# Optimization experiments

Hardware: AMD Instinct MI355X
Metric: run time of the kernel (lower is better)

The kernel has to match this reference:

```python
import jax, jax.numpy as jnp
import numpy as np


def _bilinear_align_corners(img, H_out, W_out):
    # img: [B, C, h, w] -> [B, C, H_out, W_out], matching F.interpolate(mode='bilinear', align_corners=True)
    b, c, h, w = img.shape
    ys = jnp.linspace(0.0, h - 1.0, H_out)
    xs = jnp.linspace(0.0, w - 1.0, W_out)
    y0 = jnp.floor(ys).astype(jnp.int32)
    x0 = jnp.floor(xs).astype(jnp.int32)
    y1 = jnp.minimum(y0 + 1, h - 1)
    x1 = jnp.minimum(x0 + 1, w - 1)
    wy = (ys - y0)[:, None]          # [H_out, 1]
    wx = (xs - x0)[None, :]          # [1, W_out]

    def gather(yi, xi):
        return img[:, :, yi, :][:, :, :, xi]  # [B, C, H_out, W_out]

    top = gather(y0, x0) * (1.0 - wx) + gather(y0, x1) * wx
    bot = gather(y1, x0) * (1.0 - wx) + gather(y1, x1) * wx
    return top * (1.0 - wy) + bot * wy


def _conv1x1(x, W, b):
    # x: [B, C, H, W_], W: [O, C], b: [O]
    return jnp.einsum('bchw,oc->bohw', x, W) + b[None, :, None, None]


def setup_inputs() -> dict:
    key = jax.random.key(0)
    ks = jax.random.split(key, 9)
    B, C, H, W = 4, 256, 64, 64
    C8 = C // 8
    s_qk = 1.0 / np.sqrt(C)
    return {
        'x': jax.random.normal(ks[0], (B, C, H, W), dtype=jnp.float32),
        'guiding_map0': jax.random.normal(ks[1], (B, 1, 32, 32), dtype=jnp.float32),
        'Wq': jax.random.normal(ks[2], (C8, C), dtype=jnp.float32) * s_qk,
        'bq': jax.random.normal(ks[3], (C8,), dtype=jnp.float32) * 0.01,
        'Wk': jax.random.normal(ks[4], (C8, C), dtype=jnp.float32) * s_qk,
        'bk': jax.random.normal(ks[5], (C8,), dtype=jnp.float32) * 0.01,
        'Wv': jax.random.normal(ks[6], (C, C), dtype=jnp.float32) * s_qk,
        'bv': jax.random.normal(ks[7], (C,), dtype=jnp.float32) * 0.01,
        'gamma': jax.random.normal(ks[8], (1,), dtype=jnp.float32) * 0.1,
    }


def reference(x, guiding_map0, Wq, bq, Wk, bk, Wv, bv, gamma):
    B, C, H, W = x.shape
    N = H * W
    # upsample guiding map to x's spatial size, then sigmoid gate
    gm = jax.nn.sigmoid(_bilinear_align_corners(guiding_map0, H, W))  # [B,1,H,W]
    gate = 1.0 + gm

    q = (_conv1x1(x, Wq, bq) * gate).reshape(B, -1, N)  # [B, C//8, N]
    k = (_conv1x1(x, Wk, bk) * gate).reshape(B, -1, N)  # [B, C//8, N]
    v = (_conv1x1(x, Wv, bv) * gate).reshape(B, C, N)   # [B, C, N]

    # energy[b, n, m] = q[b, :, n] . k[b, :, m]
    energy = jnp.einsum('bcn,bcm->bnm', q, k)           # [B, N, N]
    attention = jax.nn.softmax(energy, axis=-1)
    # out[b, c, n] = sum_m v[b, c, m] * attention[b, n, m]
    out = jnp.einsum('bcm,bnm->bcn', v, attention).reshape(B, C, H, W)
    return gamma[0] * out + x
```

## Files before the change

kernel.cpp:

```cpp
#include <hip/hip_runtime.h>
#include <hip/hip_bf16.h>
#include <cstdint>

typedef __attribute__((ext_vector_type(4)))  float f32x4;
typedef __attribute__((ext_vector_type(16))) float f32x16;
typedef __attribute__((ext_vector_type(8)))  short s16x8;

#define LOG2E 1.4426950408889634f
#define MFIX  64.0f

#define B_   4
#define C_   256
#define N_   4096
#define NT_  256
#define MB_  128
#define QG_  128

#define WS_WFRAG 0u
#define WS_BIAS  163840u
#define WS_Q     262144u
#define WS_K     1310720u
#define WS_V     2359296u
#define WS_PART  11534336u
#define WS_ML    45088768u
#define WS_NEED  45613056ull

__device__ __forceinline__ short bf16s(float f) {
  return (short)__bfloat16_as_ushort(__float2bfloat16(f));
}
__device__ __forceinline__ float bf2f(short h) {
  union { unsigned u; float f; } v; v.u = ((unsigned)(unsigned short)h) << 16;
  return v.f;
}
__device__ __forceinline__ void gl_lds16(const void* g, void* l) {
  __builtin_amdgcn_global_load_lds(
      (const __attribute__((address_space(1))) unsigned int*)g,
      (__attribute__((address_space(3))) unsigned int*)l, 16, 0, 0);
}

__global__ void wprep_kernel(const float* __restrict__ Wq, const float* __restrict__ Wk,
                             const float* __restrict__ Wv, const float* __restrict__ bq,
                             const float* __restrict__ bk, const float* __restrict__ bv,
                             short* __restrict__ wfrag, float* __restrict__ bias) {
  int d0 = blockIdx.x * 256 + threadIdx.x;
  int d = d0;
  int j  = d & 7;  d >>= 3;
  int c  = d & 15; d >>= 4;
  int g  = d & 3;  d >>= 2;
  int ks = d & 7;  d >>= 3;
  int t  = d;
  int o  = t * 16 + c;
  int ch = ks * 32 + g * 8 + j;
  float w = (o < 32) ? Wq[o * 256 + ch] : (o < 64) ? Wk[(o - 32) * 256 + ch]
                                                   : Wv[(o - 64) * 256 + ch];
  wfrag[d0] = bf16s(w);
  if (d0 < 320) bias[d0] = (d0 < 32) ? bq[d0] : (d0 < 64) ? bk[d0 - 32] : bv[d0 - 64];
}

__global__ __launch_bounds__(256) void proj_kernel(
    const float* __restrict__ x, const short* __restrict__ wfrag,
    const float* __restrict__ bias, const float* __restrict__ gm,
    short* __restrict__ qs, short* __restrict__ ksz, short* __restrict__ vs) {
  int b = blockIdx.x >> 8, nt = blockIdx.x & 255;
  int lane = threadIdx.x & 63, wave = threadIdx.x >> 6;
  int g = lane >> 4, c = lane & 15;
  int n = nt * 16 + c;

  float gt;
  {
    int y = n >> 6, xp = n & 63;
    float fy = (float)(y * 31) / 63.0f;
    float fx = (float)(xp * 31) / 63.0f;
    int y0 = (int)fy, x0 = (int)fx;
    float wy = fy - (float)y0, wx = fx - (float)x0;
    int y1 = min(y0 + 1, 31), x1 = min(x0 + 1, 31);
    const float* p = gm + b * 1024;
    float v00 = p[y0 * 32 + x0], v01 = p[y0 * 32 + x1];
    float v10 = p[y1 * 32 + x0], v11 = p[y1 * 32 + x1];
    float top = v00 * (1.f - wx) + v01 * wx;
    float bot = v10 * (1.f - wx) + v11 * wx;
    float gv  = top * (1.f - wy) + bot * wy;
    gt = 1.0f + 1.0f / (1.0f + expf(-gv));
  }

  const float* xb = x + b * (C_ * N_) + n;
  s16x8 xf[8];
  #pragma unroll
  for (int ks = 0; ks < 8; ++ks) {
    int ch0 = ks * 32 + g * 8;
    s16x8 v;
    #pragma unroll
    for (int j = 0; j < 8; ++j) v[j] = bf16s(xb[(ch0 + j) * N_]);
    xf[ks] = v;
  }

  int qt32 = n >> 5, r = n & 31;
  for (int t = wave * 5; t < wave * 5 + 5; ++t) {
    f32x4 acc = {0.f, 0.f, 0.f, 0.f};
    #pragma unroll
    for (int ks = 0; ks < 8; ++ks) {
      s16x8 wf = *(const s16x8*)(wfrag + ((((t * 8 + ks) * 4 + g) * 16 + c) * 8));
      acc = __builtin_amdgcn_mfma_f32_16x16x32_bf16(wf, xf[ks], acc, 0, 0, 0);
    }
    #pragma unroll
    for (int jj = 0; jj < 4; ++jj) {
      int o = t * 16 + g * 4 + jj;
      float val = (acc[jj] + bias[o]) * gt;
      short bv16 = bf16s(val);
      if (o < 64) {
        int ch = o & 31;
        int s  = (ch >> 4) & 1, hi = (ch >> 3) & 1, j = ch & 7;
        short* dst = (o < 32) ? qs : ksz;
        dst[(((b * QG_ + qt32) * 2 + s) * 64 + hi * 32 + r) * 8 + j] = bv16;
      } else {
        int cv = o - 64;
        int ct = cv >> 5, lam = cv & 31;
        int s  = (r >> 4) & 1, r4 = r & 15;
        int k  = (r4 & 3) | (((r4 >> 3) & 1) << 2) | (((r4 >> 2) & 1) << 3);
        int hi = k >> 3, j = k & 7;
        vs[((((size_t)(b * MB_ + qt32) * 8 + ct) * 2 + s) * 64 + hi * 32 + lam) * 8 + j] = bv16;
      }
    }
  }
}

__global__ __launch_bounds__(256, 4) void attn_split_kernel(
    const short* __restrict__ qs, const short* __restrict__ ksz,
    const short* __restrict__ vs, short* __restrict__ part,
    float* __restrict__ mlbuf) {
  __shared__ __align__(16) short k_lds[4][1024];
  __shared__ __align__(16) short v_lds[4][4096];

  int bid = blockIdx.x;
  int b  = (bid & 7) >> 1;
  int u  = ((bid >> 3) << 1) | (bid & 1);
  int h  = u & 1;
  int s  = (u >> 1) & 3;
  int qb = u >> 3;
  int tid = threadIdx.x, lane = tid & 63, wave = tid >> 6;
  int lq = lane & 31, hi = lane >> 5;
  int qt = qb * 4 + wave;

  const short* qbp = qs + (size_t)(((b * QG_ + qt) * 2) * 64 + lane) * 8;
  s16x8 qf0 = *(const s16x8*)(qbp);
  s16x8 qf1 = *(const s16x8*)(qbp + 512);
  asm volatile("s_waitcnt vmcnt(0)" ::: "memory");

  f32x16 acc[4];
  #pragma unroll
  for (int ct = 0; ct < 4; ++ct)
    #pragma unroll
    for (int e = 0; e < 16; ++e) acc[ct][e] = 0.f;
  float lsum = 0.f;

  const char* kbase = (const char*)(ksz + (size_t)b * (MB_ * 1024));
  const char* vbase = (const char*)(vs + (size_t)b * ((size_t)MB_ * 8192));

  #define STAGE(mb, nb)                                                          \
    {                                                                            \
      const char* vsrc = vbase + (size_t)(mb) * 16384 + h * 8192;                \
      gl_lds16(vsrc + tid * 16,        &v_lds[nb][tid * 8]);                     \
      gl_lds16(vsrc + 4096 + tid * 16, &v_lds[nb][2048 + tid * 8]);              \
      if (tid < 128) {                                                           \
        const char* ksrc = kbase + (size_t)(mb) * 2048;                          \
        gl_lds16(ksrc + tid * 16, &k_lds[nb][tid * 8]);                          \
      }                                                                          \
    }
  #define WAIT_PREV()                                                            \
    {                                                                            \
      if (wave < 2) asm volatile("s_waitcnt vmcnt(3)" ::: "memory");             \
      else          asm volatile("s_waitcnt vmcnt(2)" ::: "memory");             \
    }

  s16x8 pf0, pf1;
  f32x16 st;

  #define QKT(buf)                                                               \
    {                                                                            \
      const short* kb = k_lds[buf];                                              \
      s16x8 kf0 = *(const s16x8*)(kb + lane * 8);                                \
      s16x8 kf1 = *(const s16x8*)(kb + 512 + lane * 8);                          \
      _Pragma("unroll")                                                          \
      for (int e = 0; e < 16; ++e) st[e] = 0.f;                                  \
      st = __builtin_amdgcn_mfma_f32_32x32x16_bf16(kf0, qf0, st, 0, 0, 0);       \
      st = __builtin_amdgcn_mfma_f32_32x32x16_bf16(kf1, qf1, st, 0, 0, 0);       \
    }

  #define SOFTMAX()                                                              \
    {                                                                            \
      float psum = 0.f;                                                          \
      _Pragma("unroll")                                                          \
      for (int j = 0; j < 8; ++j) {                                              \
        float p = exp2f((st[j] - MFIX) * LOG2E);                                 \
        psum += p; pf0[j] = bf16s(p);                                            \
      }                                                                          \
      _Pragma("unroll")                                                          \
      for (int j = 0; j < 8; ++j) {                                              \
        float p = exp2f((st[8 + j] - MFIX) * LOG2E);                             \
        psum += p; pf1[j] = bf16s(p);                                            \
      }                                                                          \
      lsum += psum;                                                              \
    }

  #define PVACC(buf)                                                             \
    {                                                                            \
      const short* vb = v_lds[buf];                                              \
      _Pragma("unroll")                                                          \
      for (int ct = 0; ct < 4; ++ct) {                                           \
        s16x8 vf0 = *(const s16x8*)(vb + (ct * 2 + 0) * 512 + lane * 8);         \
        s16x8 vf1 = *(const s16x8*)(vb + (ct * 2 + 1) * 512 + lane * 8);         \
        acc[ct] = __builtin_amdgcn_mfma_f32_32x32x16_bf16(vf0, pf0, acc[ct], 0, 0, 0); \
        acc[ct] = __builtin_amdgcn_mfma_f32_32x32x16_bf16(vf1, pf1, acc[ct], 0, 0, 0); \
      }                                                                          \
    }

  int base = s * 32;
  STAGE(base + 0, 0);
  {
    STAGE(base + 1, 1);
    WAIT_PREV();
    __builtin_amdgcn_s_barrier();
    QKT(0);
    SOFTMAX();
  }
  for (int j = 1; j < 32; ++j) {
    int jn = (j + 1 > 31) ? 31 : j + 1;
    STAGE(base + jn, (j + 1) & 3);
    WAIT_PREV();
    __builtin_amdgcn_s_barrier();
    __builtin_amdgcn_s_setprio(1);
    QKT(j & 3);
    PVACC((j - 1) & 3);
    __builtin_amdgcn_s_setprio(0);
    SOFTMAX();
  }
  PVACC(31 & 3);

  lsum += __shfl_xor(lsum, 32);

  int pt = (b * 128 + qt) * 4 + s;
  if (lane < 32) mlbuf[pt * 64 + lq] = lsum;
  short* pb = part + (size_t)pt * 8192 + h * 4096;
  #pragma unroll
  for (int ct = 0; ct < 4; ++ct)
    #pragma unroll
    for (int e = 0; e < 16; ++e) {
      int CH = ct * 32 + (e & 3) + 8 * (e >> 2) + 4 * hi;
      pb[CH * 32 + lq] = bf16s(acc[ct][e]);
    }
  #undef STAGE
  #undef WAIT_PREV
  #undef QKT
  #undef SOFTMAX
  #undef PVACC
}

__global__ __launch_bounds__(256) void combine_kernel(
    const short* __restrict__ part, const float* __restrict__ mlbuf,
    const float* __restrict__ x, const float* __restrict__ gamma,
    float* __restrict__ out) {
  int bid = blockIdx.x;
  int b = bid >> 7, qt = bid & 127;
  int t = threadIdx.x;
  int q = t & 31, cg = t >> 5;
  int base = (b * 128 + qt) * 4;
  float L = mlbuf[(base + 0) * 64 + q] + mlbuf[(base + 1) * 64 + q]
          + mlbuf[(base + 2) * 64 + q] + mlbuf[(base + 3) * 64 + q];
  float rn = gamma[0] / L;
  int n = qt * 32 + q;
  const short* p0 = part + (size_t)(base + 0) * 8192;
  const short* p1 = part + (size_t)(base + 1) * 8192;
  const short* p2 = part + (size_t)(base + 2) * 8192;
  const short* p3 = part + (size_t)(base + 3) * 8192;
  #pragma unroll 4
  for (int cc = 0; cc < 32; ++cc) {
    int ch = cg * 32 + cc;
    int off = ch * 32 + q;
    float o = bf2f(p0[off]) + bf2f(p1[off]) + bf2f(p2[off]) + bf2f(p3[off]);
    int idx = (b * C_ + ch) * N_ + n;
    out[idx] = rn * o + x[idx];
  }
}

__global__ __launch_bounds__(256, 2) void attn_reg_kernel(
    const short* __restrict__ qs, const short* __restrict__ ksz,
    const short* __restrict__ vs, const float* __restrict__ x,
    const float* __restrict__ gamma, float* __restrict__ out) {
  __shared__ float comb_l[4][32];
  __shared__ float sumbuf[4][16][4][64];

  int bid = blockIdx.x;
  int b  = (bid & 7) >> 1;
  int qg = ((bid >> 3) << 1) | (bid & 1);
  int tid = threadIdx.x, lane = tid & 63, wave = tid >> 6;
  int lq = lane & 31;

  const short* qb = qs + (size_t)(((b * QG_ + qg) * 2) * 64 + lane) * 8;
  s16x8 qf0 = *(const s16x8*)(qb);
  s16x8 qf1 = *(const s16x8*)(qb + 512);

  f32x16 acc[8];
  #pragma unroll
  for (int ct = 0; ct < 8; ++ct)
    #pragma unroll
    for (int e = 0; e < 16; ++e) acc[ct][e] = 0.f;
  float lsum = 0.f;

  const short* kb0 = ksz + (size_t)b * (MB_ * 1024) + lane * 8;
  const short* vb0 = vs  + (size_t)b * ((size_t)MB_ * 8192) + lane * 8;

  int mb = wave;
  s16x8 kf0 = *(const s16x8*)(kb0 + mb * 1024);
  s16x8 kf1 = *(const s16x8*)(kb0 + mb * 1024 + 512);

  for (int i = 0; i < 32; ++i) {
    const short* vb = vb0 + (size_t)mb * 8192;
    s16x8 vf[16];
    #pragma unroll
    for (int t = 0; t < 16; ++t) vf[t] = *(const s16x8*)(vb + t * 512);

    f32x16 st;
    #pragma unroll
    for (int e = 0; e < 16; ++e) st[e] = 0.f;
    st = __builtin_amdgcn_mfma_f32_32x32x16_bf16(kf0, qf0, st, 0, 0, 0);
    st = __builtin_amdgcn_mfma_f32_32x32x16_bf16(kf1, qf1, st, 0, 0, 0);

    int mbn = (i < 31) ? (mb + 4) : wave;
    s16x8 nk0 = *(const s16x8*)(kb0 + mbn * 1024);
    s16x8 nk1 = *(const s16x8*)(kb0 + mbn * 1024 + 512);

    float psum = 0.f;
    s16x8 pf0, pf1;
    #pragma unroll
    for (int j = 0; j < 8; ++j) {
      float p = exp2f((st[j] - MFIX) * LOG2E);
      psum += p; pf0[j] = bf16s(p);
    }
    #pragma unroll
    for (int j = 0; j < 8; ++j) {
      float p = exp2f((st[8 + j] - MFIX) * LOG2E);
      psum += p; pf1[j] = bf16s(p);
    }
    lsum += psum;

    #pragma unroll
    for (int ct = 0; ct < 8; ++ct) {
      acc[ct] = __builtin_amdgcn_mfma_f32_32x32x16_bf16(vf[ct * 2],     pf0, acc[ct], 0, 0, 0);
      acc[ct] = __builtin_amdgcn_mfma_f32_32x32x16_bf16(vf[ct * 2 + 1], pf1, acc[ct], 0, 0, 0);
    }
    kf0 = nk0; kf1 = nk1; mb = mbn;
  }

  lsum += __shfl_xor(lsum, 32);
  if (lane < 32) comb_l[wave][lq] = lsum;
  __syncthreads();
  float L = comb_l[0][lq] + comb_l[1][lq] + comb_l[2][lq] + comb_l[3][lq];
  float rn = gamma[0] / L;
  int n = qg * 32 + lq;
  int hi = lane >> 5;

  for (int phase = 0; phase < 2; ++phase) {
    #pragma unroll
    for (int t = 0; t < 4; ++t)
      #pragma unroll
      for (int e = 0; e < 16; ++e)
        sumbuf[t][e][wave][lane] = acc[phase * 4 + t][e];
    __syncthreads();
    int ct = phase * 4 + wave;
    #pragma unroll
    for (int e = 0; e < 16; ++e) {
      float ssum = sumbuf[wave][e][0][lane] + sumbuf[wave][e][1][lane]
                 + sumbuf[wave][e][2][lane] + sumbuf[wave][e][3][lane];
      int ch = ct * 32 + (e & 3) + 8 * (e >> 2) + 4 * hi;
      int idx = (b * C_ + ch) * N_ + n;
      out[idx] = rn * ssum + x[idx];
    }
    __syncthreads();
  }
}

extern "C" void kernel_launch(void* const* d_in, const int* in_sizes, int n_in,
                              void* d_out, int out_size, void* d_ws, size_t ws_size,
                              hipStream_t stream) {
  const float* x     = (const float*)d_in[0];
  const float* gm    = (const float*)d_in[1];
  const float* Wq    = (const float*)d_in[2];
  const float* bq    = (const float*)d_in[3];
  const float* Wk    = (const float*)d_in[4];
  const float* bk    = (const float*)d_in[5];
  const float* Wv    = (const float*)d_in[6];
  const float* bv    = (const float*)d_in[7];
  const float* gamma = (const float*)d_in[8];

  char*  ws    = (char*)d_ws;
  short* wfrag = (short*)(ws + WS_WFRAG);
  float* bias  = (float*)(ws + WS_BIAS);
  short* qs    = (short*)(ws + WS_Q);
  short* ksz   = (short*)(ws + WS_K);
  short* vs    = (short*)(ws + WS_V);
  float* out   = (float*)d_out;

  wprep_kernel<<<dim3(320), dim3(256), 0, stream>>>(Wq, Wk, Wv, bq, bk, bv, wfrag, bias);
  proj_kernel<<<dim3(1024), dim3(256), 0, stream>>>(x, wfrag, bias, gm, qs, ksz, vs);

  if (ws_size >= WS_NEED) {
    short* part  = (short*)(ws + WS_PART);
    float* mlbuf = (float*)(ws + WS_ML);
    attn_split_kernel<<<dim3(1024), dim3(256), 0, stream>>>(qs, ksz, vs, part, mlbuf);
    combine_kernel<<<dim3(512), dim3(256), 0, stream>>>(part, mlbuf, x, gamma, out);
  } else {
    attn_reg_kernel<<<dim3(512), dim3(256), 0, stream>>>(qs, ksz, vs, x, gamma, out);
  }
}
```

Measured before the change: 99.26 us.

## Share QK^T softmax across channel-half waves via LDS in attention split kernel

Merges the two channel-half blocks into one 512-thread block, so each query tile's QK^T and exp are computed once by the h==0 wave. The resulting probabilities are passed through a double-buffered LDS buffer to the h==1 wave. K staging is no longer duplicated across blocks, and V for both halves is staged together with a 3-deep ring. The cost is load imbalance, since h==0 waves do QK^T plus softmax while h==1 waves only do PV, plus extra barriers, LDS traffic and larger shared memory use that may lower occupancy.

After: 100.2 us. About the same (+0.9%).

```diff
diff --git a/kernel.cpp b/kernel.cpp
--- a/kernel.cpp
+++ b/kernel.cpp
@@ -124,22 +124,22 @@
   }
 }
 
-__global__ __launch_bounds__(256, 4) void attn_split_kernel(
+__global__ __launch_bounds__(512, 4) void attn_split_kernel(
     const short* __restrict__ qs, const short* __restrict__ ksz,
     const short* __restrict__ vs, short* __restrict__ part,
     float* __restrict__ mlbuf) {
-  __shared__ __align__(16) short k_lds[4][1024];
-  __shared__ __align__(16) short v_lds[4][4096];
+  __shared__ __align__(16) short k_lds[3][1024];
+  __shared__ __align__(16) short v_lds[3][8192];
+  __shared__ __align__(16) short p_lds[2][4][2][512];
 
   int bid = blockIdx.x;
   int b  = (bid & 7) >> 1;
   int u  = ((bid >> 3) << 1) | (bid & 1);
-  int h  = u & 1;
-  int s  = (u >> 1) & 3;
-  int qb = u >> 3;
+  int qb = u >> 2, s = u & 3;
   int tid = threadIdx.x, lane = tid & 63, wave = tid >> 6;
+  int qi = wave >> 1, h = wave & 1;
   int lq = lane & 31, hi = lane >> 5;
-  int qt = qb * 4 + wave;
+  int qt = qb * 4 + qi;
 
   const short* qbp = qs + (size_t)(((b * QG_ + qt) * 2) * 64 + lane) * 8;
   s16x8 qf0 = *(const s16x8*)(qbp);
@@ -158,9 +158,9 @@
 
   #define STAGE(mb, nb)                                                          \
     {                                                                            \
-      const char* vsrc = vbase + (size_t)(mb) * 16384 + h * 8192;                \
+      const char* vsrc = vbase + (size_t)(mb) * 16384;                           \
       gl_lds16(vsrc + tid * 16,        &v_lds[nb][tid * 8]);                     \
-      gl_lds16(vsrc + 4096 + tid * 16, &v_lds[nb][2048 + tid * 8]);              \
+      gl_lds16(vsrc + 8192 + tid * 16, &v_lds[nb][4096 + tid * 8]);              \
       if (tid < 128) {                                                           \
         const char* ksrc = kbase + (size_t)(mb) * 2048;                          \
         gl_lds16(ksrc + tid * 16, &k_lds[nb][tid * 8]);                          \
@@ -171,8 +171,11 @@
       if (wave < 2) asm volatile("s_waitcnt vmcnt(3)" ::: "memory");             \
       else          asm volatile("s_waitcnt vmcnt(2)" ::: "memory");             \
     }
+  #define BARRIER_LGKM() asm volatile("s_waitcnt lgkmcnt(0)\n\ts_barrier" ::: "memory")
+  #define BARRIER_RAW()  asm volatile("s_barrier" ::: "memory")
 
   s16x8 pf0, pf1;
+  s16x8 ps0, ps1;
   f32x16 st;
 
   #define QKT(buf)                                                               \
@@ -192,66 +195,95 @@
       _Pragma("unroll")                                                          \
       for (int j = 0; j < 8; ++j) {                                              \
         float p = exp2f((st[j] - MFIX) * LOG2E);                                 \
-        psum += p; pf0[j] = bf16s(p);                                            \
+        psum += p; ps0[j] = bf16s(p);                                            \
       }                                                                          \
       _Pragma("unroll")                                                          \
       for (int j = 0; j < 8; ++j) {                                              \
         float p = exp2f((st[8 + j] - MFIX) * LOG2E);                             \
-        psum += p; pf1[j] = bf16s(p);                                            \
+        psum += p; ps1[j] = bf16s(p);                                            \
       }                                                                          \
       lsum += psum;                                                              \
     }
 
+  #define PREAD(jpar)                                                            \
+    {                                                                            \
+      pf0 = *(const s16x8*)&p_lds[jpar][qi][0][lane * 8];                        \
+      pf1 = *(const s16x8*)&p_lds[jpar][qi][1][lane * 8];                        \
+    }
+  #define PWRITE(jpar)                                                           \
+    {                                                                            \
+      *(s16x8*)&p_lds[jpar][qi][0][lane * 8] = ps0;                              \
+      *(s16x8*)&p_lds[jpar][qi][1][lane * 8] = ps1;                              \
+    }
+
   #define PVACC(buf)                                                             \
     {                                                                            \
-      const short* vb = v_lds[buf];                                              \
+      const short* vb = v_lds[buf] + h * 4096;                                   \
       _Pragma("unroll")                                                          \
-      for (int ct = 0; ct < 4; ++ct) {                                           \
-        s16x8 vf0 = *(const s16x8*)(vb + (ct * 2 + 0) * 512 + lane * 8);         \
-        s16x8 vf1 = *(const s16x8*)(vb + (ct * 2 + 1) * 512 + lane * 8);         \
-        acc[ct] = __builtin_amdgcn_mfma_f32_32x32x16_bf16(vf0, pf0, acc[ct], 0, 0, 0); \
-        acc[ct] = __builtin_amdgcn_mfma_f32_32x32x16_bf16(vf1, pf1, acc[ct], 0, 0, 0); \
+      for (int ctl = 0; ctl < 4; ++ctl) {                                        \
+        s16x8 vf0 = *(const s16x8*)(vb + (ctl * 2 + 0) * 512 + lane * 8);        \
+        s16x8 vf1 = *(const s16x8*)(vb + (ctl * 2 + 1) * 512 + lane * 8);        \
+        acc[ctl] = __builtin_amdgcn_mfma_f32_32x32x16_bf16(vf0, pf0, acc[ctl], 0, 0, 0); \
+        acc[ctl] = __builtin_amdgcn_mfma_f32_32x32x16_bf16(vf1, pf1, acc[ctl], 0, 0, 0); \
       }                                                                          \
     }
 
   int base = s * 32;
   STAGE(base + 0, 0);
-  {
-    STAGE(base + 1, 1);
-    WAIT_PREV();
-    __builtin_amdgcn_s_barrier();
+  STAGE(base + 1, 1);
+  WAIT_PREV();
+  BARRIER_LGKM();
+  if (h == 0) {
     QKT(0);
     SOFTMAX();
-  }
-  for (int j = 1; j < 32; ++j) {
-    int jn = (j + 1 > 31) ? 31 : j + 1;
-    STAGE(base + jn, (j + 1) & 3);
+    PWRITE(0);
+  }
+
+  int bc = 0, bn = 1, bs = 2;
+  for (int j = 0; j < 32; ++j) {
+    BARRIER_LGKM();
+    int jn = j + 2; if (jn > 31) jn = 31;
+    STAGE(base + jn, bs);
     WAIT_PREV();
-    __builtin_amdgcn_s_barrier();
-    __builtin_amdgcn_s_setprio(1);
-    QKT(j & 3);
-    PVACC((j - 1) & 3);
-    __builtin_amdgcn_s_setprio(0);
-    SOFTMAX();
-  }
-  PVACC(31 & 3);
+    BARRIER_RAW();
+    PREAD(j & 1);
+    if (h == 0) {
+      __builtin_amdgcn_s_setprio(1);
+      if (j < 31) QKT(bn);
+      PVACC(bc);
+      __builtin_amdgcn_s_setprio(0);
+      if (j < 31) {
+        SOFTMAX();
+        PWRITE((j + 1) & 1);
+      }
+    } else {
+      __builtin_amdgcn_s_setprio(1);
+      PVACC(bc);
+      __builtin_amdgcn_s_setprio(0);
+    }
+    int t = bc; bc = bn; bn = bs; bs = t;
+  }
 
   lsum += __shfl_xor(lsum, 32);
 
   int pt = (b * 128 + qt) * 4 + s;
-  if (lane < 32) mlbuf[pt * 64 + lq] = lsum;
+  if (h == 0 && lane < 32) mlbuf[pt * 64 + lq] = lsum;
   short* pb = part + (size_t)pt * 8192 + h * 4096;
   #pragma unroll
-  for (int ct = 0; ct < 4; ++ct)
+  for (int ctl = 0; ctl < 4; ++ctl)
     #pragma unroll
     for (int e = 0; e < 16; ++e) {
-      int CH = ct * 32 + (e & 3) + 8 * (e >> 2) + 4 * hi;
-      pb[CH * 32 + lq] = bf16s(acc[ct][e]);
+      int CH = ctl * 32 + (e & 3) + 8 * (e >> 2) + 4 * hi;
+      pb[CH * 32 + lq] = bf16s(acc[ctl][e]);
     }
   #undef STAGE
   #undef WAIT_PREV
+  #undef BARRIER_LGKM
+  #undef BARRIER_RAW
   #undef QKT
   #undef SOFTMAX
+  #undef PREAD
+  #undef PWRITE
   #undef PVACC
 }
 
@@ -406,7 +438,7 @@
   if (ws_size >= WS_NEED) {
     short* part  = (short*)(ws + WS_PART);
     float* mlbuf = (float*)(ws + WS_ML);
-    attn_split_kernel<<<dim3(1024), dim3(256), 0, stream>>>(qs, ksz, vs, part, mlbuf);
+    attn_split_kernel<<<dim3(512), dim3(512), 0, stream>>>(qs, ksz, vs, part, mlbuf);
     combine_kernel<<<dim3(512), dim3(256), 0, stream>>>(part, mlbuf, x, gamma, out);
   } else {
     attn_reg_kernel<<<dim3(512), dim3(256), 0, stream>>>(qs, ksz, vs, x, gamma, out);
```
